# Optimization experiments

Measured on AMD Instinct MI355X. Metric: run time of the kernel, lower is better.

The kernel has to match this reference:

```python
import jax, jax.numpy as jnp
import numpy as np

SEQ, BATCH, D_IN, D_OUT, LATENT = 2048, 32, 256, 256, 64


def setup_inputs() -> dict:
    key = jax.random.key(0)
    k1, k2, k3, k4 = jax.random.split(key, 4)
    x = jax.random.normal(k1, (SEQ, BATCH, D_IN), dtype=jnp.float32)
    # Scale A so spectral radius < 1: raw uniform(64,64) would make the 2048-step
    # recurrence blow up to inf; stable A is required for a usable baseline.
    A = jax.random.uniform(k2, (LATENT, LATENT), dtype=jnp.float32) * (0.9 / LATENT)
    B = jax.random.normal(k3, (LATENT, D_IN), dtype=jnp.float32) * 0.05
    C = jax.random.normal(k4, (D_OUT, LATENT), dtype=jnp.float32) * 0.05
    return {"x": x, "A": A, "B": B, "C": C}


def reference(x, A, B, C):
    # x: [S, B, D_in]; SSM recurrence h[t+1] = A h[t] + B x[t], y[t] = C h[t+1]
    S, Bt, _ = x.shape
    L = A.shape[0]
    # Precompute input projections for all timesteps at once: [S, B, L]
    bx = jnp.einsum('sbd,ld->sbl', x, B)
    h0 = jnp.zeros((Bt, L), dtype=x.dtype)

    def step(h, u):
        h_new = h @ A.T + u  # [B, L]
        return h_new, h_new

    _, hs = jax.lax.scan(step, h0, bx)            # hs: [S, B, L]
    h = jnp.concatenate([h0[None], hs], axis=0)   # [S+1, B, L] (includes h[0])
    y = jnp.einsum('sbl,ol->sbo', hs, C)          # [S, B, D_out]
    return y, h
```

## Files before the change

### kernel.cpp

```cpp
#include <hip/hip_runtime.h>
#include <stdint.h>

#define SEQ  2048
#define NBAT 32
#define DIN  256
#define DOUT 256
#define LAT  64
#define CH   32
#define WARM 16

typedef __attribute__((ext_vector_type(8))) short short8;
typedef __attribute__((ext_vector_type(4))) float f32x4;

__device__ __forceinline__ float bf2f(unsigned short u) {
  return __uint_as_float(((unsigned int)u) << 16);
}
__device__ __forceinline__ unsigned short f2bf(float f) {
  unsigned int u = __float_as_uint(f);
  u += 0x7fffu + ((u >> 16) & 1u);
  return (unsigned short)(u >> 16);
}
__device__ __forceinline__ unsigned int pack2bf(float lo, float hi) {
  unsigned int a = __float_as_uint(lo);
  unsigned int b = __float_as_uint(hi);
  a += 0x7fffu + ((a >> 16) & 1u);
  b += 0x7fffu + ((b >> 16) & 1u);
  return (a >> 16) | (b & 0xffff0000u);
}

#define PACK8(DST, VA, VB) { \
    union { unsigned int u[4]; short8 s; } _r; \
    _r.u[0] = pack2bf((VA)[0], (VA)[1]); \
    _r.u[1] = pack2bf((VA)[2], (VA)[3]); \
    _r.u[2] = pack2bf((VB)[0], (VB)[1]); \
    _r.u[3] = pack2bf((VB)[2], (VB)[3]); \
    DST = _r.s; }

#define XDECL(P) f32x4 P##0a,P##0b,P##1a,P##1b,P##2a,P##2b,P##3a,P##3b, \
                       P##4a,P##4b,P##5a,P##5b,P##6a,P##6b,P##7a,P##7b;
#define XLD(P,K,R) { const float* _xp = X + (size_t)((R) + m) * 256 + (K)*32 + q*8; \
    P##K##a = *(const f32x4*)_xp;  P##K##b = *(const f32x4*)(_xp + 4); }
#define XLDALL(P,R) XLD(P,0,R) XLD(P,1,R) XLD(P,2,R) XLD(P,3,R) \
                    XLD(P,4,R) XLD(P,5,R) XLD(P,6,R) XLD(P,7,R)
#define BXK(P,K) { short8 _a; PACK8(_a, P##K##a, P##K##b); \
    short8 _b0 = *(const short8*)(Bl8 + ((K)*4+0)*512 + lane*8); \
    short8 _b1 = *(const short8*)(Bl8 + ((K)*4+1)*512 + lane*8); \
    short8 _b2 = *(const short8*)(Bl8 + ((K)*4+2)*512 + lane*8); \
    short8 _b3 = *(const short8*)(Bl8 + ((K)*4+3)*512 + lane*8); \
    acc0 = __builtin_amdgcn_mfma_f32_16x16x32_bf16(_a, _b0, acc0, 0, 0, 0); \
    acc1 = __builtin_amdgcn_mfma_f32_16x16x32_bf16(_a, _b1, acc1, 0, 0, 0); \
    acc2 = __builtin_amdgcn_mfma_f32_16x16x32_bf16(_a, _b2, acc2, 0, 0, 0); \
    acc3 = __builtin_amdgcn_mfma_f32_16x16x32_bf16(_a, _b3, acc3, 0, 0, 0); }
#define BXTILE(P,R) { \
    f32x4 acc0={0,0,0,0}, acc1={0,0,0,0}, acc2={0,0,0,0}, acc3={0,0,0,0}; \
    BXK(P,0) BXK(P,1) BXK(P,2) BXK(P,3) BXK(P,4) BXK(P,5) BXK(P,6) BXK(P,7) \
    _Pragma("unroll") \
    for (int r = 0; r < 4; ++r) { \
      unsigned short* _op = bxh + (size_t)((R) + q*4 + r) * 64 + m; \
      _op[ 0] = f2bf(acc0[r]);  _op[16] = f2bf(acc1[r]); \
      _op[32] = f2bf(acc2[r]);  _op[48] = f2bf(acc3[r]); } }

__global__ __launch_bounds__(256) void k_bx(const float* __restrict__ X,
                                            const float* __restrict__ Bm,
                                            unsigned short* __restrict__ bxh,
                                            float* __restrict__ hout) {
  __shared__ unsigned int Bl[8192];
  const int tid = threadIdx.x;
  if (blockIdx.x < 8) hout[blockIdx.x * 256 + tid] = 0.0f;

#pragma unroll
  for (int ii = 0; ii < 32; ++ii) {
    const int i  = ii * 256 + tid;
    const int w  = i & 3, ln = (i >> 2) & 63, f = i >> 8;
    const int kc = f >> 2, nt = f & 3;
    const int row = nt * 16 + (ln & 15);
    const int col = kc * 32 + (ln >> 4) * 8 + w * 2;
    const float* p = Bm + row * 256 + col;
    Bl[i] = pack2bf(p[0], p[1]);
  }
  __syncthreads();

  const int lane = tid & 63;
  const int m = lane & 15, q = lane >> 4;
  const unsigned short* Bl8 = (const unsigned short*)Bl;
  const int wid = blockIdx.x * 4 + (tid >> 6);
  const int R0  = wid * 32;

  XDECL(Xa) XDECL(Xb)
  XLDALL(Xa, R0)
  XLDALL(Xb, R0 + 16)
  BXTILE(Xa, R0)
  BXTILE(Xb, R0 + 16)
}

#define YMF(NT) { \
    short8 _f0 = *(const short8*)(Cl8 + ( 0 + NT)*512 + lane*8); \
    short8 _f1 = *(const short8*)(Cl8 + (16 + NT)*512 + lane*8); \
    C##NT = __builtin_amdgcn_mfma_f32_16x16x32_bf16(Af0, _f0, C##NT, 0, 0, 0); \
    C##NT = __builtin_amdgcn_mfma_f32_16x16x32_bf16(Af1, _f1, C##NT, 0, 0, 0); }
#define YST(NT) { \
    float* _yp = Y + ((size_t)(tb + TIL*16 + q*4) * 32 + b) * 256 + NT*16 + m; \
    _yp[0] = C##NT[0]; _yp[8192] = C##NT[1]; _yp[16384] = C##NT[2]; _yp[24576] = C##NT[3]; }
#define YTILE(TIL) { \
    short8 Af0 = *(const short8*)(hw + (TIL*16 + m)*72 +  0 + q*8); \
    short8 Af1 = *(const short8*)(hw + (TIL*16 + m)*72 + 32 + q*8); \
    f32x4 C0={0,0,0,0},C1={0,0,0,0},C2={0,0,0,0},C3={0,0,0,0}, \
          C4={0,0,0,0},C5={0,0,0,0},C6={0,0,0,0},C7={0,0,0,0}, \
          C8={0,0,0,0},C9={0,0,0,0},C10={0,0,0,0},C11={0,0,0,0}, \
          C12={0,0,0,0},C13={0,0,0,0},C14={0,0,0,0},C15={0,0,0,0}; \
    YMF(0) YMF(1) YMF(2) YMF(3) YMF(4) YMF(5) YMF(6) YMF(7) \
    YMF(8) YMF(9) YMF(10) YMF(11) YMF(12) YMF(13) YMF(14) YMF(15) \
    YST(0) YST(1) YST(2) YST(3) YST(4) YST(5) YST(6) YST(7) \
    YST(8) YST(9) YST(10) YST(11) YST(12) YST(13) YST(14) YST(15) }

__global__ __launch_bounds__(256) void k_rec_y(const float* __restrict__ Amat,
                                               const unsigned short* __restrict__ bxh,
                                               float* __restrict__ hout,
                                               const float* __restrict__ Cm,
                                               float* __restrict__ Y) {
  __shared__ unsigned int Cl[8192];
  __shared__ __align__(16) unsigned short hlds[4 * 32 * 72];
  const int tid = threadIdx.x;

#pragma unroll
  for (int ii = 0; ii < 32; ++ii) {
    const int i  = ii * 256 + tid;
    const int w  = i & 3, ln = (i >> 2) & 63, f = i >> 8;
    const int s  = f >> 4, nt = f & 15;
    const int row = nt * 16 + (ln & 15);
    const int col = s * 32 + (ln >> 4) * 8 + w * 2;
    const float* p = Cm + row * 64 + col;
    Cl[i] = pack2bf(p[0], p[1]);
  }
  __syncthreads();

  const int lane = tid & 63;
  const int wv   = tid >> 6;
  const int wid  = blockIdx.x * 4 + wv;
  const int c    = wid >> 5;
  const int b    = wid & 31;
  unsigned short* hw = hlds + wv * (32 * 72);

  const f32x4* Ap = (const f32x4*)(Amat + lane * 64);
  const f32x4 A0 = Ap[0],  A1 = Ap[1],  A2 = Ap[2],  A3 = Ap[3];
  const f32x4 A4 = Ap[4],  A5 = Ap[5],  A6 = Ap[6],  A7 = Ap[7];
  const f32x4 A8 = Ap[8],  A9 = Ap[9],  A10 = Ap[10], A11 = Ap[11];
  const f32x4 A12 = Ap[12], A13 = Ap[13], A14 = Ap[14], A15 = Ap[15];

  int tstart = c * CH - WARM;
  if (tstart < 0) tstart = 0;
  const int tout = c * CH;

  const unsigned short* up = bxh + (size_t)tstart * (NBAT * LAT) + b * LAT + lane;
  float c0 = bf2f(up[0]);
  float c1 = bf2f(up[2048]);
  float c2 = bf2f(up[4096]);
  float c3 = bf2f(up[6144]);
  up += 8192;

  float h = 0.0f;

#define RL(K) __uint_as_float(__builtin_amdgcn_readlane(hu, (K)))
#define G4(V, K) \
    h0 = fmaf(V[0], RL(K+0), h0); \
    h1 = fmaf(V[1], RL(K+1), h1); \
    h2 = fmaf(V[2], RL(K+2), h2); \
    h3 = fmaf(V[3], RL(K+3), h3);
#define STEP(UU) { \
    const unsigned int hu = __float_as_uint(h); \
    float h0 = (UU), h1 = 0.f, h2 = 0.f, h3 = 0.f; \
    G4(A0,  0) G4(A1,  4) G4(A2,  8) G4(A3, 12) \
    G4(A4, 16) G4(A5, 20) G4(A6, 24) G4(A7, 28) \
    G4(A8, 32) G4(A9, 36) G4(A10,40) G4(A11,44) \
    G4(A12,48) G4(A13,52) G4(A14,56) G4(A15,60) \
    h = (h0 + h1) + (h2 + h3); }

  const int warmG = (tout - tstart) >> 2;
  for (int g = 0; g < warmG; ++g) {
    float n0 = bf2f(up[0]), n1 = bf2f(up[2048]), n2 = bf2f(up[4096]), n3 = bf2f(up[6144]);
    up += 8192;
    STEP(c0) STEP(c1) STEP(c2) STEP(c3)
    c0 = n0; c1 = n1; c2 = n2; c3 = n3;
  }

  float* hp = hout + (size_t)(tout + 1) * (NBAT * LAT) + b * LAT + lane;
  for (int g = 0; g < 8; ++g) {
    float n0 = bf2f(up[0]), n1 = bf2f(up[2048]), n2 = bf2f(up[4096]), n3 = bf2f(up[6144]);
    up += 8192;
    STEP(c0) hp[0]    = h;  hw[(g*4+0)*72 + lane] = f2bf(h);
    STEP(c1) hp[2048] = h;  hw[(g*4+1)*72 + lane] = f2bf(h);
    STEP(c2) hp[4096] = h;  hw[(g*4+2)*72 + lane] = f2bf(h);
    STEP(c3) hp[6144] = h;  hw[(g*4+3)*72 + lane] = f2bf(h);
    hp += 8192;
    c0 = n0; c1 = n1; c2 = n2; c3 = n3;
  }
#undef STEP
#undef G4
#undef RL

  const int m = lane & 15, q = lane >> 4;
  const unsigned short* Cl8 = (const unsigned short*)Cl;
  const int tb = c * CH;
  { const int TIL = 0; YTILE(0) }
  { const int TIL = 1; YTILE(1) }
}

extern "C" void kernel_launch(void* const* d_in, const int* in_sizes, int n_in,
                              void* d_out, int out_size, void* d_ws, size_t ws_size,
                              hipStream_t stream) {
  const float* X  = (const float*)d_in[0];
  const float* Am = (const float*)d_in[1];
  const float* Bm = (const float*)d_in[2];
  const float* Cm = (const float*)d_in[3];

  float* Yout = (float*)d_out;
  float* Hout = Yout + (size_t)SEQ * NBAT * DOUT;
  unsigned short* bxh = (unsigned short*)d_ws;

  k_bx   <<<512, 256, 0, stream>>>(X, Bm, bxh, Hout);
  k_rec_y<<<512, 256, 0, stream>>>(Am, bxh, Hout, Cm, Yout);
}
```

Measured before the change: 169.0 us.

## Fuse input projection into recurrence kernel, computing Bx per wave in LDS

Merges the separate Bx projection kernel into the recurrence/output kernel. Each wave now computes its own 48-timestep Bx slice (warmup plus chunk) with MFMA directly into LDS, so the bf16 Bx workspace is never written to or read from global memory and one launch is removed. B and C share one LDS buffer in turn, and the last step group is peeled so the prefetch never reads past the 48 staged rows. The cost is that X rows in the warmup overlap are loaded and projected twice, which raises global X traffic. LDS use per block also grows, which may reduce occupancy.

```diff
diff --git a/kernel.cpp b/kernel.cpp
--- a/kernel.cpp
+++ b/kernel.cpp
@@ -36,13 +36,11 @@
     _r.u[3] = pack2bf((VB)[2], (VB)[3]); \
     DST = _r.s; }
 
-#define XDECL(P) f32x4 P##0a,P##0b,P##1a,P##1b,P##2a,P##2b,P##3a,P##3b, \
-                       P##4a,P##4b,P##5a,P##5b,P##6a,P##6b,P##7a,P##7b;
-#define XLD(P,K,R) { const float* _xp = X + (size_t)((R) + m) * 256 + (K)*32 + q*8; \
-    P##K##a = *(const f32x4*)_xp;  P##K##b = *(const f32x4*)(_xp + 4); }
-#define XLDALL(P,R) XLD(P,0,R) XLD(P,1,R) XLD(P,2,R) XLD(P,3,R) \
-                    XLD(P,4,R) XLD(P,5,R) XLD(P,6,R) XLD(P,7,R)
-#define BXK(P,K) { short8 _a; PACK8(_a, P##K##a, P##K##b); \
+#define XDECL f32x4 x0a,x0b,x1a,x1b,x2a,x2b,x3a,x3b,x4a,x4b,x5a,x5b,x6a,x6b,x7a,x7b;
+#define FXLD(K, MT) { \
+    const float* _xp = X + (size_t)(base + (MT)*16 + m) * 8192 + b * 256 + (K)*32 + q*8; \
+    x##K##a = *(const f32x4*)_xp;  x##K##b = *(const f32x4*)(_xp + 4); }
+#define FBXK(K) { short8 _a; PACK8(_a, x##K##a, x##K##b); \
     short8 _b0 = *(const short8*)(Bl8 + ((K)*4+0)*512 + lane*8); \
     short8 _b1 = *(const short8*)(Bl8 + ((K)*4+1)*512 + lane*8); \
     short8 _b2 = *(const short8*)(Bl8 + ((K)*4+2)*512 + lane*8); \
@@ -51,20 +49,44 @@
     acc1 = __builtin_amdgcn_mfma_f32_16x16x32_bf16(_a, _b1, acc1, 0, 0, 0); \
     acc2 = __builtin_amdgcn_mfma_f32_16x16x32_bf16(_a, _b2, acc2, 0, 0, 0); \
     acc3 = __builtin_amdgcn_mfma_f32_16x16x32_bf16(_a, _b3, acc3, 0, 0, 0); }
-#define BXTILE(P,R) { \
+#define FTILE(MT) { \
+    FXLD(0,MT) FXLD(1,MT) FXLD(2,MT) FXLD(3,MT) \
+    FXLD(4,MT) FXLD(5,MT) FXLD(6,MT) FXLD(7,MT) \
     f32x4 acc0={0,0,0,0}, acc1={0,0,0,0}, acc2={0,0,0,0}, acc3={0,0,0,0}; \
-    BXK(P,0) BXK(P,1) BXK(P,2) BXK(P,3) BXK(P,4) BXK(P,5) BXK(P,6) BXK(P,7) \
+    FBXK(0) FBXK(1) FBXK(2) FBXK(3) FBXK(4) FBXK(5) FBXK(6) FBXK(7) \
     _Pragma("unroll") \
     for (int r = 0; r < 4; ++r) { \
-      unsigned short* _op = bxh + (size_t)((R) + q*4 + r) * 64 + m; \
+      unsigned short* _op = bxw + ((MT)*16 + q*4 + r) * 72 + m; \
       _op[ 0] = f2bf(acc0[r]);  _op[16] = f2bf(acc1[r]); \
       _op[32] = f2bf(acc2[r]);  _op[48] = f2bf(acc3[r]); } }
 
-__global__ __launch_bounds__(256) void k_bx(const float* __restrict__ X,
-                                            const float* __restrict__ Bm,
-                                            unsigned short* __restrict__ bxh,
-                                            float* __restrict__ hout) {
-  __shared__ unsigned int Bl[8192];
+#define YMF(NT) { \
+    short8 _f0 = *(const short8*)(Cl8 + ( 0 + NT)*512 + lane*8); \
+    short8 _f1 = *(const short8*)(Cl8 + (16 + NT)*512 + lane*8); \
+    C##NT = __builtin_amdgcn_mfma_f32_16x16x32_bf16(Af0, _f0, C##NT, 0, 0, 0); \
+    C##NT = __builtin_amdgcn_mfma_f32_16x16x32_bf16(Af1, _f1, C##NT, 0, 0, 0); }
+#define YST(NT) { \
+    float* _yp = Y + ((size_t)(tb + TIL*16 + q*4) * 32 + b) * 256 + NT*16 + m; \
+    _yp[0] = C##NT[0]; _yp[8192] = C##NT[1]; _yp[16384] = C##NT[2]; _yp[24576] = C##NT[3]; }
+#define YTILE(TILARG) { \
+    short8 Af0 = *(const short8*)(hw + (TILARG*16 + m)*72 +  0 + q*8); \
+    short8 Af1 = *(const short8*)(hw + (TILARG*16 + m)*72 + 32 + q*8); \
+    f32x4 C0={0,0,0,0},C1={0,0,0,0},C2={0,0,0,0},C3={0,0,0,0}, \
+          C4={0,0,0,0},C5={0,0,0,0},C6={0,0,0,0},C7={0,0,0,0}, \
+          C8={0,0,0,0},C9={0,0,0,0},C10={0,0,0,0},C11={0,0,0,0}, \
+          C12={0,0,0,0},C13={0,0,0,0},C14={0,0,0,0},C15={0,0,0,0}; \
+    YMF(0) YMF(1) YMF(2) YMF(3) YMF(4) YMF(5) YMF(6) YMF(7) \
+    YMF(8) YMF(9) YMF(10) YMF(11) YMF(12) YMF(13) YMF(14) YMF(15) \
+    YST(0) YST(1) YST(2) YST(3) YST(4) YST(5) YST(6) YST(7) \
+    YST(8) YST(9) YST(10) YST(11) YST(12) YST(13) YST(14) YST(15) }
+
+__global__ __launch_bounds__(256) void k_fused(
+    const float* __restrict__ X, const float* __restrict__ Amat,
+    const float* __restrict__ Bm, const float* __restrict__ Cm,
+    float* __restrict__ hout, float* __restrict__ Y) {
+  __shared__ __align__(16) unsigned int BCl[8192];
+  __shared__ __align__(16) unsigned short bxl[4 * 48 * 72];
+  __shared__ __align__(16) unsigned short hlds[4 * 32 * 72];
   const int tid = threadIdx.x;
   if (blockIdx.x < 8) hout[blockIdx.x * 256 + tid] = 0.0f;
 
@@ -76,51 +98,24 @@
     const int row = nt * 16 + (ln & 15);
     const int col = kc * 32 + (ln >> 4) * 8 + w * 2;
     const float* p = Bm + row * 256 + col;
-    Bl[i] = pack2bf(p[0], p[1]);
+    BCl[i] = pack2bf(p[0], p[1]);
   }
   __syncthreads();
 
   const int lane = tid & 63;
-  const int m = lane & 15, q = lane >> 4;
-  const unsigned short* Bl8 = (const unsigned short*)Bl;
-  const int wid = blockIdx.x * 4 + (tid >> 6);
-  const int R0  = wid * 32;
-
-  XDECL(Xa) XDECL(Xb)
-  XLDALL(Xa, R0)
-  XLDALL(Xb, R0 + 16)
-  BXTILE(Xa, R0)
-  BXTILE(Xb, R0 + 16)
-}
-
-#define YMF(NT) { \
-    short8 _f0 = *(const short8*)(Cl8 + ( 0 + NT)*512 + lane*8); \
-    short8 _f1 = *(const short8*)(Cl8 + (16 + NT)*512 + lane*8); \
-    C##NT = __builtin_amdgcn_mfma_f32_16x16x32_bf16(Af0, _f0, C##NT, 0, 0, 0); \
-    C##NT = __builtin_amdgcn_mfma_f32_16x16x32_bf16(Af1, _f1, C##NT, 0, 0, 0); }
-#define YST(NT) { \
-    float* _yp = Y + ((size_t)(tb + TIL*16 + q*4) * 32 + b) * 256 + NT*16 + m; \
-    _yp[0] = C##NT[0]; _yp[8192] = C##NT[1]; _yp[16384] = C##NT[2]; _yp[24576] = C##NT[3]; }
-#define YTILE(TIL) { \
-    short8 Af0 = *(const short8*)(hw + (TIL*16 + m)*72 +  0 + q*8); \
-    short8 Af1 = *(const short8*)(hw + (TIL*16 + m)*72 + 32 + q*8); \
-    f32x4 C0={0,0,0,0},C1={0,0,0,0},C2={0,0,0,0},C3={0,0,0,0}, \
-          C4={0,0,0,0},C5={0,0,0,0},C6={0,0,0,0},C7={0,0,0,0}, \
-          C8={0,0,0,0},C9={0,0,0,0},C10={0,0,0,0},C11={0,0,0,0}, \
-          C12={0,0,0,0},C13={0,0,0,0},C14={0,0,0,0},C15={0,0,0,0}; \
-    YMF(0) YMF(1) YMF(2) YMF(3) YMF(4) YMF(5) YMF(6) YMF(7) \
-    YMF(8) YMF(9) YMF(10) YMF(11) YMF(12) YMF(13) YMF(14) YMF(15) \
-    YST(0) YST(1) YST(2) YST(3) YST(4) YST(5) YST(6) YST(7) \
-    YST(8) YST(9) YST(10) YST(11) YST(12) YST(13) YST(14) YST(15) }
-
-__global__ __launch_bounds__(256) void k_rec_y(const float* __restrict__ Amat,
-                                               const unsigned short* __restrict__ bxh,
-                                               float* __restrict__ hout,
-                                               const float* __restrict__ Cm,
-                                               float* __restrict__ Y) {
-  __shared__ unsigned int Cl[8192];
-  __shared__ __align__(16) unsigned short hlds[4 * 32 * 72];
-  const int tid = threadIdx.x;
+  const int wv   = tid >> 6;
+  const int wid  = blockIdx.x * 4 + wv;
+  const int c    = wid >> 5;
+  const int b    = wid & 31;
+  const int m    = lane & 15, q = lane >> 4;
+  const int tout = c * CH;
+  int base = tout - WARM; if (base < 0) base = 0;
+  unsigned short* bxw = bxl + wv * (48 * 72);
+  const unsigned short* Bl8 = (const unsigned short*)BCl;
+
+  { XDECL
+    FTILE(0) FTILE(1) FTILE(2) }
+  __syncthreads();
 
 #pragma unroll
   for (int ii = 0; ii < 32; ++ii) {
@@ -130,33 +125,24 @@
     const int row = nt * 16 + (ln & 15);
     const int col = s * 32 + (ln >> 4) * 8 + w * 2;
     const float* p = Cm + row * 64 + col;
-    Cl[i] = pack2bf(p[0], p[1]);
+    BCl[i] = pack2bf(p[0], p[1]);
   }
   __syncthreads();
 
-  const int lane = tid & 63;
-  const int wv   = tid >> 6;
-  const int wid  = blockIdx.x * 4 + wv;
-  const int c    = wid >> 5;
-  const int b    = wid & 31;
   unsigned short* hw = hlds + wv * (32 * 72);
-
   const f32x4* Ap = (const f32x4*)(Amat + lane * 64);
   const f32x4 A0 = Ap[0],  A1 = Ap[1],  A2 = Ap[2],  A3 = Ap[3];
   const f32x4 A4 = Ap[4],  A5 = Ap[5],  A6 = Ap[6],  A7 = Ap[7];
   const f32x4 A8 = Ap[8],  A9 = Ap[9],  A10 = Ap[10], A11 = Ap[11];
   const f32x4 A12 = Ap[12], A13 = Ap[13], A14 = Ap[14], A15 = Ap[15];
 
-  int tstart = c * CH - WARM;
-  if (tstart < 0) tstart = 0;
-  const int tout = c * CH;
-
-  const unsigned short* up = bxh + (size_t)tstart * (NBAT * LAT) + b * LAT + lane;
+  const int warmG = (tout - base) >> 2;
+  const unsigned short* up = bxw + lane;
   float c0 = bf2f(up[0]);
-  float c1 = bf2f(up[2048]);
-  float c2 = bf2f(up[4096]);
-  float c3 = bf2f(up[6144]);
-  up += 8192;
+  float c1 = bf2f(up[72]);
+  float c2 = bf2f(up[144]);
+  float c3 = bf2f(up[216]);
+  up += 288;
 
   float h = 0.0f;
 
@@ -175,18 +161,17 @@
     G4(A12,48) G4(A13,52) G4(A14,56) G4(A15,60) \
     h = (h0 + h1) + (h2 + h3); }
 
-  const int warmG = (tout - tstart) >> 2;
   for (int g = 0; g < warmG; ++g) {
-    float n0 = bf2f(up[0]), n1 = bf2f(up[2048]), n2 = bf2f(up[4096]), n3 = bf2f(up[6144]);
-    up += 8192;
+    float n0 = bf2f(up[0]), n1 = bf2f(up[72]), n2 = bf2f(up[144]), n3 = bf2f(up[216]);
+    up += 288;
     STEP(c0) STEP(c1) STEP(c2) STEP(c3)
     c0 = n0; c1 = n1; c2 = n2; c3 = n3;
   }
 
   float* hp = hout + (size_t)(tout + 1) * (NBAT * LAT) + b * LAT + lane;
-  for (int g = 0; g < 8; ++g) {
-    float n0 = bf2f(up[0]), n1 = bf2f(up[2048]), n2 = bf2f(up[4096]), n3 = bf2f(up[6144]);
-    up += 8192;
+  for (int g = 0; g < 7; ++g) {
+    float n0 = bf2f(up[0]), n1 = bf2f(up[72]), n2 = bf2f(up[144]), n3 = bf2f(up[216]);
+    up += 288;
     STEP(c0) hp[0]    = h;  hw[(g*4+0)*72 + lane] = f2bf(h);
     STEP(c1) hp[2048] = h;  hw[(g*4+1)*72 + lane] = f2bf(h);
     STEP(c2) hp[4096] = h;  hw[(g*4+2)*72 + lane] = f2bf(h);
@@ -194,13 +179,16 @@
     hp += 8192;
     c0 = n0; c1 = n1; c2 = n2; c3 = n3;
   }
+  STEP(c0) hp[0]    = h;  hw[28*72 + lane] = f2bf(h);
+  STEP(c1) hp[2048] = h;  hw[29*72 + lane] = f2bf(h);
+  STEP(c2) hp[4096] = h;  hw[30*72 + lane] = f2bf(h);
+  STEP(c3) hp[6144] = h;  hw[31*72 + lane] = f2bf(h);
 #undef STEP
 #undef G4
 #undef RL
 
-  const int m = lane & 15, q = lane >> 4;
-  const unsigned short* Cl8 = (const unsigned short*)Cl;
-  const int tb = c * CH;
+  const unsigned short* Cl8 = (const unsigned short*)BCl;
+  const int tb = tout;
   { const int TIL = 0; YTILE(0) }
   { const int TIL = 1; YTILE(1) }
 }
@@ -215,8 +203,7 @@
 
   float* Yout = (float*)d_out;
   float* Hout = Yout + (size_t)SEQ * NBAT * DOUT;
-  unsigned short* bxh = (unsigned short*)d_ws;
-
-  k_bx   <<<512, 256, 0, stream>>>(X, Bm, bxh, Hout);
-  k_rec_y<<<512, 256, 0, stream>>>(Am, bxh, Hout, Cm, Yout);
-}
+  (void)d_ws; (void)ws_size;
+
+  k_fused<<<512, 256, 0, stream>>>(X, Am, Bm, Cm, Hout, Yout);
+}
```

Result: slower. 176.7 us (+4.6%).

## Run recurrence with MFMA across batch and split Y projection into own kernel

Applied to the files above, without the earlier changes.

The scalar readlane/FMA recurrence, where each wave handled one batch element, becomes MFMA matrix steps. Each wave now handles 16 batch elements, and the hidden state is kept in split hi/lo bf16 form, exchanged through LDS, to preserve precision. The chunk length drops from 32 to 16, giving 256 single-wave blocks. A bf16 copy of h goes to a workspace, and a separate k_y kernel computes the C projection from it. The aim is to cut per-step latency on the serial chain, at the cost of an extra launch, extra global traffic, and a higher share of warmup steps.

```diff
diff --git a/kernel.cpp b/kernel.cpp
--- a/kernel.cpp
+++ b/kernel.cpp
@@ -3,14 +3,14 @@
 
 #define SEQ  2048
 #define NBAT 32
-#define DIN  256
-#define DOUT 256
 #define LAT  64
-#define CH   32
+#define CH   16
 #define WARM 16
 
 typedef __attribute__((ext_vector_type(8))) short short8;
 typedef __attribute__((ext_vector_type(4))) float f32x4;
+typedef __attribute__((ext_vector_type(4))) unsigned short us4;
+typedef __attribute__((ext_vector_type(2))) unsigned int uint2e;
 
 __device__ __forceinline__ float bf2f(unsigned short u) {
   return __uint_as_float(((unsigned int)u) << 16);
@@ -93,17 +93,110 @@
   BXTILE(Xb, R0 + 16)
 }
 
+#define MSTEP(AF0, AF1, DD) \
+    DD = __builtin_amdgcn_mfma_f32_16x16x32_bf16(AF0, Bhi0, DD, 0, 0, 0); \
+    DD = __builtin_amdgcn_mfma_f32_16x16x32_bf16(AF1, Bhi1, DD, 0, 0, 0); \
+    DD = __builtin_amdgcn_mfma_f32_16x16x32_bf16(AF0, Blo0, DD, 0, 0, 0); \
+    DD = __builtin_amdgcn_mfma_f32_16x16x32_bf16(AF1, Blo1, DD, 0, 0, 0);
+
+#define SPLIT(MI, DD) \
+    const unsigned int hh##MI##_0 = pack2bf(DD[0], DD[1]); \
+    const unsigned int hh##MI##_1 = pack2bf(DD[2], DD[3]); \
+    { float _f0 = __uint_as_float(hh##MI##_0 << 16); \
+      float _f1 = __uint_as_float(hh##MI##_0 & 0xffff0000u); \
+      float _f2 = __uint_as_float(hh##MI##_1 << 16); \
+      float _f3 = __uint_as_float(hh##MI##_1 & 0xffff0000u); \
+      unsigned int _l01 = (__float_as_uint(DD[0] - _f0) >> 16) | \
+                          (__float_as_uint(DD[1] - _f1) & 0xffff0000u); \
+      unsigned int _l23 = (__float_as_uint(DD[2] - _f2) >> 16) | \
+                          (__float_as_uint(DD[3] - _f3) & 0xffff0000u); \
+      wptr[2*(MI)]     = hh##MI##_0;  wptr[2*(MI)+1]   = hh##MI##_1; \
+      wptr[8+2*(MI)]   = _l01;        wptr[8+2*(MI)+1] = _l23; }
+
+#define RDB(KB, BH, BL) { \
+    const unsigned int* _r0 = &bounce[32*(q&1) + m][2*(2*(KB) + (q>>1))]; \
+    const unsigned int* _r1 = _r0 + 16*18; \
+    union { unsigned int u[4]; short8 s; } _h, _l; \
+    *(uint2e*)&_h.u[0] = *(const uint2e*)_r0; \
+    *(uint2e*)&_h.u[2] = *(const uint2e*)_r1; \
+    *(uint2e*)&_l.u[0] = *(const uint2e*)(_r0 + 8); \
+    *(uint2e*)&_l.u[2] = *(const uint2e*)(_r1 + 8); \
+    BH = _h.s; BL = _l.s; }
+
+#define RSTEP(T, STORE) { \
+    us4 un0, un1, un2, un3; \
+    { const unsigned short* _p = ub + (size_t)((T) + 1) * 2048; \
+      un0 = *(const us4*)(_p);      un1 = *(const us4*)(_p + 16); \
+      un2 = *(const us4*)(_p + 32); un3 = *(const us4*)(_p + 48); } \
+    f32x4 D0 = {bf2f(uc0[0]), bf2f(uc0[1]), bf2f(uc0[2]), bf2f(uc0[3])}; \
+    f32x4 D1 = {bf2f(uc1[0]), bf2f(uc1[1]), bf2f(uc1[2]), bf2f(uc1[3])}; \
+    f32x4 D2 = {bf2f(uc2[0]), bf2f(uc2[1]), bf2f(uc2[2]), bf2f(uc2[3])}; \
+    f32x4 D3 = {bf2f(uc3[0]), bf2f(uc3[1]), bf2f(uc3[2]), bf2f(uc3[3])}; \
+    MSTEP(Af00, Af01, D0) MSTEP(Af10, Af11, D1) \
+    MSTEP(Af20, Af21, D2) MSTEP(Af30, Af31, D3) \
+    if (STORE) { \
+      float* _hp = hout + ((size_t)(T) + 1) * 2048 + b * 64 + 4 * q; \
+      *(f32x4*)(_hp)      = D0;  *(f32x4*)(_hp + 16) = D1; \
+      *(f32x4*)(_hp + 32) = D2;  *(f32x4*)(_hp + 48) = D3; } \
+    SPLIT(0, D0) SPLIT(1, D1) SPLIT(2, D2) SPLIT(3, D3) \
+    if (STORE) { \
+      unsigned int* _hb = (unsigned int*)(hbf + (size_t)(T) * 2048 + b * 64 + 4 * q); \
+      _hb[0]  = hh0_0; _hb[1]  = hh0_1;  _hb[8]  = hh1_0; _hb[9]  = hh1_1; \
+      _hb[16] = hh2_0; _hb[17] = hh2_1;  _hb[24] = hh3_0; _hb[25] = hh3_1; } \
+    RDB(0, Bhi0, Blo0) RDB(1, Bhi1, Blo1) \
+    uc0 = un0; uc1 = un1; uc2 = un2; uc3 = un3; }
+
+__global__ __launch_bounds__(64) void k_rec(const float* __restrict__ Amat,
+                                            const unsigned short* __restrict__ bxh,
+                                            float* __restrict__ hout,
+                                            unsigned short* __restrict__ hbf) {
+  __shared__ unsigned int bounce[64][18];
+  const int lane = threadIdx.x;
+  const int wid  = blockIdx.x;
+  const int c    = wid >> 1;
+  const int g    = wid & 1;
+  const int q    = lane >> 4, m = lane & 15;
+  const int b    = g * 16 + m;
+  unsigned int* wptr = &bounce[lane][0];
+
+  short8 Af00, Af01, Af10, Af11, Af20, Af21, Af30, Af31;
+#define LDA(MI, KB, DST) { \
+    const float* _ap = Amat + (16*(MI) + m) * 64 + 32*(KB) + 8*q; \
+    f32x4 _a = *(const f32x4*)_ap; f32x4 _c = *(const f32x4*)(_ap + 4); \
+    PACK8(DST, _a, _c); }
+  LDA(0,0,Af00) LDA(0,1,Af01) LDA(1,0,Af10) LDA(1,1,Af11)
+  LDA(2,0,Af20) LDA(2,1,Af21) LDA(3,0,Af30) LDA(3,1,Af31)
+#undef LDA
+
+  short8 Bhi0 = {0,0,0,0,0,0,0,0}, Bhi1 = {0,0,0,0,0,0,0,0};
+  short8 Blo0 = {0,0,0,0,0,0,0,0}, Blo1 = {0,0,0,0,0,0,0,0};
+
+  const int tout = c * CH;
+  int t0 = tout - WARM; if (t0 < 0) t0 = 0;
+  const unsigned short* ub = bxh + (size_t)b * LAT + 4 * q;
+
+  us4 uc0, uc1, uc2, uc3;
+  { const unsigned short* _p = ub + (size_t)t0 * 2048;
+    uc0 = *(const us4*)(_p);      uc1 = *(const us4*)(_p + 16);
+    uc2 = *(const us4*)(_p + 32); uc3 = *(const us4*)(_p + 48); }
+
+  for (int t = t0; t < tout; ++t) { RSTEP(t, 0) }
+  for (int t = tout; t < tout + CH; ++t) { RSTEP(t, 1) }
+}
+
 #define YMF(NT) { \
     short8 _f0 = *(const short8*)(Cl8 + ( 0 + NT)*512 + lane*8); \
     short8 _f1 = *(const short8*)(Cl8 + (16 + NT)*512 + lane*8); \
     C##NT = __builtin_amdgcn_mfma_f32_16x16x32_bf16(Af0, _f0, C##NT, 0, 0, 0); \
     C##NT = __builtin_amdgcn_mfma_f32_16x16x32_bf16(Af1, _f1, C##NT, 0, 0, 0); }
 #define YST(NT) { \
-    float* _yp = Y + ((size_t)(tb + TIL*16 + q*4) * 32 + b) * 256 + NT*16 + m; \
-    _yp[0] = C##NT[0]; _yp[8192] = C##NT[1]; _yp[16384] = C##NT[2]; _yp[24576] = C##NT[3]; }
-#define YTILE(TIL) { \
-    short8 Af0 = *(const short8*)(hw + (TIL*16 + m)*72 +  0 + q*8); \
-    short8 Af1 = *(const short8*)(hw + (TIL*16 + m)*72 + 32 + q*8); \
+    float* _yp = Y + (size_t)(R0 + TIL*16 + q*4) * 256 + NT*16 + m; \
+    _yp[0] = C##NT[0]; _yp[256] = C##NT[1]; _yp[512] = C##NT[2]; _yp[768] = C##NT[3]; }
+#define YTILE(TILARG) { \
+    const int TIL = (TILARG); \
+    const unsigned short* _hr = hbf + (size_t)(R0 + TIL*16 + m) * 64; \
+    short8 Af0 = *(const short8*)(_hr + q*8); \
+    short8 Af1 = *(const short8*)(_hr + 32 + q*8); \
     f32x4 C0={0,0,0,0},C1={0,0,0,0},C2={0,0,0,0},C3={0,0,0,0}, \
           C4={0,0,0,0},C5={0,0,0,0},C6={0,0,0,0},C7={0,0,0,0}, \
           C8={0,0,0,0},C9={0,0,0,0},C10={0,0,0,0},C11={0,0,0,0}, \
@@ -113,13 +206,10 @@
     YST(0) YST(1) YST(2) YST(3) YST(4) YST(5) YST(6) YST(7) \
     YST(8) YST(9) YST(10) YST(11) YST(12) YST(13) YST(14) YST(15) }
 
-__global__ __launch_bounds__(256) void k_rec_y(const float* __restrict__ Amat,
-                                               const unsigned short* __restrict__ bxh,
-                                               float* __restrict__ hout,
-                                               const float* __restrict__ Cm,
-                                               float* __restrict__ Y) {
+__global__ __launch_bounds__(256) void k_y(const unsigned short* __restrict__ hbf,
+                                           const float* __restrict__ Cm,
+                                           float* __restrict__ Y) {
   __shared__ unsigned int Cl[8192];
-  __shared__ __align__(16) unsigned short hlds[4 * 32 * 72];
   const int tid = threadIdx.x;
 
 #pragma unroll
@@ -135,74 +225,13 @@
   __syncthreads();
 
   const int lane = tid & 63;
-  const int wv   = tid >> 6;
-  const int wid  = blockIdx.x * 4 + wv;
-  const int c    = wid >> 5;
-  const int b    = wid & 31;
-  unsigned short* hw = hlds + wv * (32 * 72);
-
-  const f32x4* Ap = (const f32x4*)(Amat + lane * 64);
-  const f32x4 A0 = Ap[0],  A1 = Ap[1],  A2 = Ap[2],  A3 = Ap[3];
-  const f32x4 A4 = Ap[4],  A5 = Ap[5],  A6 = Ap[6],  A7 = Ap[7];
-  const f32x4 A8 = Ap[8],  A9 = Ap[9],  A10 = Ap[10], A11 = Ap[11];
-  const f32x4 A12 = Ap[12], A13 = Ap[13], A14 = Ap[14], A15 = Ap[15];
-
-  int tstart = c * CH - WARM;
-  if (tstart < 0) tstart = 0;
-  const int tout = c * CH;
-
-  const unsigned short* up = bxh + (size_t)tstart * (NBAT * LAT) + b * LAT + lane;
-  float c0 = bf2f(up[0]);
-  float c1 = bf2f(up[2048]);
-  float c2 = bf2f(up[4096]);
-  float c3 = bf2f(up[6144]);
-  up += 8192;
-
-  float h = 0.0f;
-
-#define RL(K) __uint_as_float(__builtin_amdgcn_readlane(hu, (K)))
-#define G4(V, K) \
-    h0 = fmaf(V[0], RL(K+0), h0); \
-    h1 = fmaf(V[1], RL(K+1), h1); \
-    h2 = fmaf(V[2], RL(K+2), h2); \
-    h3 = fmaf(V[3], RL(K+3), h3);
-#define STEP(UU) { \
-    const unsigned int hu = __float_as_uint(h); \
-    float h0 = (UU), h1 = 0.f, h2 = 0.f, h3 = 0.f; \
-    G4(A0,  0) G4(A1,  4) G4(A2,  8) G4(A3, 12) \
-    G4(A4, 16) G4(A5, 20) G4(A6, 24) G4(A7, 28) \
-    G4(A8, 32) G4(A9, 36) G4(A10,40) G4(A11,44) \
-    G4(A12,48) G4(A13,52) G4(A14,56) G4(A15,60) \
-    h = (h0 + h1) + (h2 + h3); }
-
-  const int warmG = (tout - tstart) >> 2;
-  for (int g = 0; g < warmG; ++g) {
-    float n0 = bf2f(up[0]), n1 = bf2f(up[2048]), n2 = bf2f(up[4096]), n3 = bf2f(up[6144]);
-    up += 8192;
-    STEP(c0) STEP(c1) STEP(c2) STEP(c3)
-    c0 = n0; c1 = n1; c2 = n2; c3 = n3;
-  }
-
-  float* hp = hout + (size_t)(tout + 1) * (NBAT * LAT) + b * LAT + lane;
-  for (int g = 0; g < 8; ++g) {
-    float n0 = bf2f(up[0]), n1 = bf2f(up[2048]), n2 = bf2f(up[4096]), n3 = bf2f(up[6144]);
-    up += 8192;
-    STEP(c0) hp[0]    = h;  hw[(g*4+0)*72 + lane] = f2bf(h);
-    STEP(c1) hp[2048] = h;  hw[(g*4+1)*72 + lane] = f2bf(h);
-    STEP(c2) hp[4096] = h;  hw[(g*4+2)*72 + lane] = f2bf(h);
-    STEP(c3) hp[6144] = h;  hw[(g*4+3)*72 + lane] = f2bf(h);
-    hp += 8192;
-    c0 = n0; c1 = n1; c2 = n2; c3 = n3;
-  }
-#undef STEP
-#undef G4
-#undef RL
-
   const int m = lane & 15, q = lane >> 4;
   const unsigned short* Cl8 = (const unsigned short*)Cl;
-  const int tb = c * CH;
-  { const int TIL = 0; YTILE(0) }
-  { const int TIL = 1; YTILE(1) }
+  const int wid = blockIdx.x * 4 + (tid >> 6);
+  const int R0  = wid * 32;
+
+  YTILE(0)
+  YTILE(1)
 }
 
 extern "C" void kernel_launch(void* const* d_in, const int* in_sizes, int n_in,
@@ -214,9 +243,11 @@
   const float* Cm = (const float*)d_in[3];
 
   float* Yout = (float*)d_out;
-  float* Hout = Yout + (size_t)SEQ * NBAT * DOUT;
+  float* Hout = Yout + (size_t)SEQ * NBAT * 256;
   unsigned short* bxh = (unsigned short*)d_ws;
-
-  k_bx   <<<512, 256, 0, stream>>>(X, Bm, bxh, Hout);
-  k_rec_y<<<512, 256, 0, stream>>>(Am, bxh, Hout, Cm, Yout);
-}
+  unsigned short* hbf = bxh + (size_t)SEQ * NBAT * LAT;
+
+  k_bx <<<512, 256, 0, stream>>>(X, Bm, bxh, Hout);
+  k_rec<<<256,  64, 0, stream>>>(Am, bxh, Hout, hbf);
+  k_y  <<<512, 256, 0, stream>>>(hbf, Cm, Yout);
+}
```

New measurement: 166.6 us. Within noise of the previous version (-1.4%).
